# Optimization experiments

Measured on AMD Instinct MI355X. Metric: run time of the kernel, lower is better.

The kernel has to match this reference:

```python
import jax, jax.numpy as jnp
import numpy as np

B, T, D = 16, 2048, 64
K = 8192


def setup_inputs() -> dict:
    key = jax.random.key(0)
    k_x, k_cb = jax.random.split(key)
    x = jax.random.normal(k_x, (B, T, D), dtype=jnp.float32)
    # codebook initialized as randn(K, D) / sqrt(D), as in EMAQuantizer.__init__
    codebook = jax.random.normal(k_cb, (K, D), dtype=jnp.float32) / jnp.sqrt(jnp.float32(D))
    return {"x": x, "codebook": codebook}


def reference(x, codebook):
    """EMAQuantizer.forward (eval mode): nearest-codebook lookup + straight-through.

    x: [B, T, D], codebook: [K, D] -> (x_q_st [B,T,D], indices [B,T])
    """
    orig_shape = x.shape
    x_flat = x.reshape(-1, x.shape[-1])                       # [N, D]
    x2 = jnp.sum(x_flat * x_flat, axis=1, keepdims=True)      # [N, 1]
    e2 = jnp.sum(codebook * codebook, axis=1)[None, :]        # [1, K]
    xe = x_flat @ codebook.T                                  # [N, K]
    dist = x2 + e2 - 2.0 * xe                                 # [N, K] squared L2
    indices = jnp.argmin(dist, axis=1)                        # [N]
    x_q = codebook[indices].reshape(orig_shape)               # gather lookup
    x_q_st = x + jax.lax.stop_gradient(x_q - x)               # straight-through
    return x_q_st, indices.reshape(orig_shape[:-1])
```

## Files before the change

### kernel.cpp

```cpp
#include <hip/hip_runtime.h>
#include <hip/hip_bf16.h>
#include <math.h>

#define N_ROWS 32768
#define KCODES 8192
#define DDIM 64

typedef __attribute__((ext_vector_type(8))) short bf16x8;
typedef __attribute__((ext_vector_type(4))) float f32x4;

#define O_XBF   0
#define O_QPERM 4194304UL
#define O_X2    5242880UL
#define O_E2    5373952UL
#define O_E2MAX 5406720UL
#define O_SLOTS 5668880UL
#define WS_NEEDED (O_SLOTS + (size_t)N_ROWS * 16 * 4)
#define CAPL 32

__device__ __forceinline__ unsigned short f2bf(float f) {
    __hip_bfloat16 h = __float2bfloat16(f);
    union { __hip_bfloat16 b; unsigned short u; } u;
    u.b = h;
    return u.u;
}

__device__ __forceinline__ float bf2f(unsigned short u) {
    return __uint_as_float(((unsigned int)u) << 16);
}

__global__ __launch_bounds__(256) void prep_kernel(const float* __restrict__ x,
                                                   const float* __restrict__ cb,
                                                   unsigned short* __restrict__ xbf,
                                                   uint4* __restrict__ qperm,
                                                   float* __restrict__ x2,
                                                   float* __restrict__ e2,
                                                   int* __restrict__ e2max_bits) {
#pragma clang fp contract(off)
    __shared__ float xrow[64][68];

    const int tid = threadIdx.x;
    const int rloc = tid >> 2;
    const int q4 = tid & 3;
    const int grow = blockIdx.x * 64 + rloc;
    const bool iscb = (grow >= N_ROWS);
    const int r = iscb ? (grow - N_ROWS) : grow;
    const float* src = iscb ? (cb + (size_t)r * DDIM) : (x + (size_t)r * DDIM);

    float4 v[4];
#pragma unroll
    for (int h2 = 0; h2 < 4; ++h2) v[h2] = ((const float4*)src)[q4 * 4 + h2];
#pragma unroll
    for (int h2 = 0; h2 < 4; ++h2)
        *(float4*)&xrow[rloc][q4 * 16 + h2 * 4] = v[h2];

    uint4 ch[2];
#pragma unroll
    for (int hh = 0; hh < 2; ++hh) {
        float4 v0 = v[hh * 2];
        float4 v1 = v[hh * 2 + 1];
        ushort4 a, b;
        a.x = f2bf(v0.x); a.y = f2bf(v0.y); a.z = f2bf(v0.z); a.w = f2bf(v0.w);
        b.x = f2bf(v1.x); b.y = f2bf(v1.y); b.z = f2bf(v1.z); b.w = f2bf(v1.w);
        union { struct { ushort4 lo, hi; } s; uint4 u; } pk;
        pk.s.lo = a; pk.s.hi = b;
        ch[hh] = pk.u;
    }
    if (!iscb) {
        uint4* dst = (uint4*)(xbf + (size_t)r * DDIM);
        dst[q4 * 2 + 0] = ch[0];
        dst[q4 * 2 + 1] = ch[1];
    } else {
        const int g = r >> 4, l15 = r & 15;
#pragma unroll
        for (int hh = 0; hh < 2; ++hh) {
            const int h = q4 * 2 + hh;
            const int slot = (g * 2 + (h >> 2)) * 64 + (h & 3) * 16 + l15;
            qperm[slot] = ch[hh];
        }
    }
    __syncthreads();

    if (tid < 64) {
        float acc[8];
#pragma unroll
        for (int j = 0; j < 8; ++j) { float vv = xrow[tid][j]; acc[j] = vv * vv; }
#pragma unroll
        for (int i = 8; i < 64; i += 8)
#pragma unroll
            for (int j = 0; j < 8; ++j) { float vv = xrow[tid][i + j]; acc[j] = acc[j] + vv * vv; }
        float s = ((acc[0] + acc[1]) + (acc[2] + acc[3])) + ((acc[4] + acc[5]) + (acc[6] + acc[7]));
        const int grow2 = blockIdx.x * 64 + tid;
        if (grow2 < N_ROWS) {
            x2[grow2] = s;
        } else {
            e2[grow2 - N_ROWS] = s;
            float wm = s;
#pragma unroll
            for (int m = 1; m < 64; m <<= 1) wm = fmaxf(wm, __shfl_xor(wm, m, 64));
            if (tid == 0) atomicMax(e2max_bits, __float_as_int(wm));
        }
    }
}

__global__ __launch_bounds__(512) void screen_fused_kernel(
    const unsigned short* __restrict__ xbf, const uint4* __restrict__ qperm,
    const float* __restrict__ xg, const float* __restrict__ cbg,
    const float* __restrict__ x2g, const float* __restrict__ e2g,
    const int* __restrict__ e2max_bits, float* __restrict__ out) {
    __shared__ float tilemax_lds[64 * 64];
    __shared__ unsigned short xs_lds[64][64];
    __shared__ unsigned int wl[4096];
    __shared__ float thr_lds[64];
    __shared__ int cnt_lds[64];
    __shared__ int slots_lds[64][CAPL];
    __shared__ int wcnt;

    const int tid = threadIdx.x;
    const int w = tid >> 6;
    const int lane = tid & 63;
    const int l15 = lane & 15;
    const int quad = lane >> 4;
    const int row0 = blockIdx.x * 64;
    const int T0 = w * 64;

    ((uint4*)xs_lds)[tid] = *((const uint4*)(xbf + (size_t)row0 * DDIM) + tid);
    if (tid == 0) wcnt = 0;
    if (tid < 64) cnt_lds[tid] = 0;

    bf16x8 afrag[4][2];
#pragma unroll
    for (int rt = 0; rt < 4; ++rt)
#pragma unroll
        for (int s = 0; s < 2; ++s)
            afrag[rt][s] = *(const bf16x8*)(xbf + (size_t)(row0 + rt * 16 + l15) * DDIM +
                                            s * 32 + quad * 8);

    const uint4* pB = qperm + (size_t)T0 * 128 + lane;
    const float* pE = e2g + T0 * 16 + l15;

    bf16x8 b0[2], b1[2];
    float ee2[2];
#pragma unroll
    for (int i = 0; i < 2; ++i) {
        b0[i] = *(const bf16x8*)(pB + (size_t)i * 128);
        b1[i] = *(const bf16x8*)(pB + (size_t)i * 128 + 64);
        ee2[i] = pE[i * 16];
    }

    float tmax[4][4];
#pragma unroll
    for (int rt = 0; rt < 4; ++rt)
#pragma unroll
        for (int reg = 0; reg < 4; ++reg) tmax[rt][reg] = -3.0e38f;

    for (int g = 0; g < 8; ++g) {
#pragma unroll 2
        for (int j = 0; j < 8; ++j) {
            const int t = g * 8 + j;
            const int buf = t & 1;
            const bf16x8 B0 = b0[buf];
            const bf16x8 B1 = b1[buf];
            const float eh = -0.5f * ee2[buf];
            if (t < 62) {
                const uint4* p = pB + (size_t)(t + 2) * 128;
                b0[buf] = *(const bf16x8*)p;
                b1[buf] = *(const bf16x8*)(p + 64);
                ee2[buf] = pE[(t + 2) * 16];
            }
            const f32x4 cin = {eh, eh, eh, eh};
#pragma unroll
            for (int rt = 0; rt < 4; ++rt) {
                f32x4 acc = __builtin_amdgcn_mfma_f32_16x16x32_bf16(afrag[rt][0], B0, cin, 0, 0, 0);
                acc = __builtin_amdgcn_mfma_f32_16x16x32_bf16(afrag[rt][1], B1, acc, 0, 0, 0);
#pragma unroll
                for (int reg = 0; reg < 4; ++reg)
                    tmax[rt][reg] = fmaxf(tmax[rt][reg], acc[reg]);
            }
        }
        const int gidx = w * 8 + g;
#pragma unroll
        for (int rt = 0; rt < 4; ++rt)
#pragma unroll
            for (int reg = 0; reg < 4; ++reg) {
                float v = tmax[rt][reg];
                v = fmaxf(v, __shfl_xor(v, 1, 64));
                v = fmaxf(v, __shfl_xor(v, 2, 64));
                v = fmaxf(v, __shfl_xor(v, 4, 64));
                v = fmaxf(v, __shfl_xor(v, 8, 64));
                if (l15 == 0) tilemax_lds[gidx * 64 + rt * 16 + quad * 4 + reg] = v;
                tmax[rt][reg] = -3.0e38f;
            }
    }
    __syncthreads();

    if (tid < 64) {
        float gs = -3.0e38f;
        for (int e = 0; e < 64; ++e) gs = fmaxf(gs, tilemax_lds[e * 64 + tid]);
        const float e2max = __int_as_float(*e2max_bits);
        thr_lds[tid] = gs - 0.005f * sqrtf(x2g[row0 + tid] * e2max) - 0.01f;
    }
    __syncthreads();

    for (int idx = tid; idx < 4096; idx += 512) {
        if (tilemax_lds[idx] >= thr_lds[idx & 63]) {
            int pos = atomicAdd(&wcnt, 1);
            wl[pos] = (unsigned int)idx;
        }
    }
    __syncthreads();

    const int nwl = wcnt;
    for (int p = w; p < nwl; p += 8) {
        const unsigned int e = wl[p];
        const int r = (int)(e & 63u);
        const int g = (int)(e >> 6);
        const float thr_r = thr_lds[r];
#pragma unroll
        for (int hh = 0; hh < 2; ++hh) {
            const int c = g * 128 + hh * 64 + lane;
            float s = -0.5f * e2g[c];
            const int cg = c >> 4, cl = c & 15;
#pragma unroll
            for (int h = 0; h < 8; ++h) {
                const int slot = (cg * 2 + (h >> 2)) * 64 + (h & 3) * 16 + cl;
                union { uint4 u; unsigned short us[8]; } qd, xd;
                qd.u = qperm[slot];
                xd.u = *(const uint4*)&xs_lds[r][h * 8];
#pragma unroll
                for (int k = 0; k < 8; ++k)
                    s = fmaf(bf2f(xd.us[k]), bf2f(qd.us[k]), s);
            }
            if (s >= thr_r) {
                int pos = atomicAdd(&cnt_lds[r], 1);
                if (pos < CAPL) slots_lds[r][pos] = c;
            }
        }
    }
    __syncthreads();

    const int sub = lane >> 3;
    const int ln8 = lane & 7;
    const int r = w * 8 + sub;
    const int row = row0 + r;
    const int c = cnt_lds[r];
    const float x2v = x2g[row];
    const float4* xv4 = (const float4*)(xg + (size_t)row * DDIM);

    float bv = 3.0e38f;
    int bi = 0x7fffffff;
    if (c <= CAPL) {
        for (int i = ln8; i < c; i += 8) {
            int code = slots_lds[r][i];
            float xe = 0.0f;
            const float4* e4 = (const float4*)(cbg + (size_t)code * DDIM);
#pragma unroll
            for (int q = 0; q < 16; ++q) {
                float4 xv = xv4[q];
                float4 ev = e4[q];
                xe = fmaf(xv.x, ev.x, xe);
                xe = fmaf(xv.y, ev.y, xe);
                xe = fmaf(xv.z, ev.z, xe);
                xe = fmaf(xv.w, ev.w, xe);
            }
            float ts = x2v + e2g[code];
            float dist = fmaf(-2.0f, xe, ts);
            if (dist < bv || (dist == bv && code < bi)) { bv = dist; bi = code; }
        }
    } else {
        for (int code = ln8; code < KCODES; code += 8) {
            float xe = 0.0f;
            const float4* e4 = (const float4*)(cbg + (size_t)code * DDIM);
#pragma unroll
            for (int q = 0; q < 16; ++q) {
                float4 xv = xv4[q];
                float4 ev = e4[q];
                xe = fmaf(xv.x, ev.x, xe);
                xe = fmaf(xv.y, ev.y, xe);
                xe = fmaf(xv.z, ev.z, xe);
                xe = fmaf(xv.w, ev.w, xe);
            }
            float ts = x2v + e2g[code];
            float dist = fmaf(-2.0f, xe, ts);
            if (dist < bv || (dist == bv && code < bi)) { bv = dist; bi = code; }
        }
    }
#pragma unroll
    for (int m = 1; m < 8; m <<= 1) {
        float ov = __shfl_xor(bv, m, 64);
        int oi = __shfl_xor(bi, m, 64);
        if (ov < bv || (ov == bv && oi < bi)) { bv = ov; bi = oi; }
    }
    {
        const float4* qs4 = (const float4*)(cbg + (size_t)bi * DDIM);
        float4* os4 = (float4*)(out + (size_t)row * DDIM);
#pragma unroll
        for (int i = 0; i < 2; ++i) {
            float4 xv = xv4[ln8 * 2 + i];
            float4 qv = qs4[ln8 * 2 + i];
            float4 ov;
            ov.x = xv.x + (qv.x - xv.x);
            ov.y = xv.y + (qv.y - xv.y);
            ov.z = xv.z + (qv.z - xv.z);
            ov.w = xv.w + (qv.w - xv.w);
            os4[ln8 * 2 + i] = ov;
        }
        if (ln8 == 0) out[(size_t)N_ROWS * DDIM + row] = (float)bi;
    }
}

#define SPLITK 4
#define KPER (KCODES / SPLITK)
#define TM 128
#define TKT 128
#define NTILES (KPER / TKT)
#define LDSX 132
#define LDSE 132

__global__ __launch_bounds__(256) void sumsq_kernel(const float* __restrict__ x,
                                                    const float* __restrict__ cb,
                                                    float* __restrict__ ws) {
#pragma clang fp contract(off)
    int t = blockIdx.x * 256 + threadIdx.x;
    const float* src;
    float* dst;
    if (t < KCODES) { src = cb + (size_t)t * DDIM; dst = ws + t; }
    else { int r = t - KCODES; src = x + (size_t)r * DDIM; dst = ws + KCODES + r; }
    float acc[8];
#pragma unroll
    for (int j = 0; j < 8; ++j) { float v = src[j]; acc[j] = v * v; }
#pragma unroll
    for (int i = 8; i < 64; i += 8)
#pragma unroll
        for (int j = 0; j < 8; ++j) { float v = src[i + j]; acc[j] = acc[j] + v * v; }
    *dst = ((acc[0] + acc[1]) + (acc[2] + acc[3])) + ((acc[4] + acc[5]) + (acc[6] + acc[7]));
}

__global__ __launch_bounds__(256) void dist_argmin_kernel(const float* __restrict__ x,
                                                          const float* __restrict__ cb,
                                                          const float* __restrict__ e2g,
                                                          const float* __restrict__ x2g,
                                                          float2* __restrict__ partial) {
    __shared__ float smem[DDIM * LDSX + DDIM * LDSE];
    float* Xs = smem;
    float* Es = smem + DDIM * LDSX;
    const int tid = threadIdx.x;
    const int row0 = blockIdx.x * TM;
    const int code0 = blockIdx.y * KPER;
    const int tr = tid >> 4, tc = tid & 15;
    for (int i = tid; i < TM * 16; i += 256) {
        int r = i >> 4, q = i & 15;
        float4 v = ((const float4*)(x + (size_t)(row0 + r) * DDIM))[q];
        Xs[(4 * q + 0) * LDSX + r] = v.x; Xs[(4 * q + 1) * LDSX + r] = v.y;
        Xs[(4 * q + 2) * LDSX + r] = v.z; Xs[(4 * q + 3) * LDSX + r] = v.w;
    }
    float x2v[8];
#pragma unroll
    for (int j = 0; j < 8; ++j) x2v[j] = x2g[row0 + tr * 8 + j];
    float bestV[8]; int bestI[8];
#pragma unroll
    for (int j = 0; j < 8; ++j) { bestV[j] = 3.0e38f; bestI[j] = 0; }
    for (int t = 0; t < NTILES; ++t) {
        __syncthreads();
        const int cbase = code0 + t * TKT;
        for (int i = tid; i < TKT * 16; i += 256) {
            int c = i >> 4, q = i & 15;
            float4 v = ((const float4*)(cb + (size_t)(cbase + c) * DDIM))[q];
            Es[(4 * q + 0) * LDSE + c] = v.x; Es[(4 * q + 1) * LDSE + c] = v.y;
            Es[(4 * q + 2) * LDSE + c] = v.z; Es[(4 * q + 3) * LDSE + c] = v.w;
        }
        __syncthreads();
        float acc[8][8];
#pragma unroll
        for (int a = 0; a < 8; ++a)
#pragma unroll
            for (int b = 0; b < 8; ++b) acc[a][b] = 0.0f;
#pragma unroll 4
        for (int d = 0; d < DDIM; ++d) {
            float xv[8], ev[8];
            float4 xa = *(const float4*)&Xs[d * LDSX + tr * 8];
            float4 xb = *(const float4*)&Xs[d * LDSX + tr * 8 + 4];
            float4 ea = *(const float4*)&Es[d * LDSE + tc * 8];
            float4 eb = *(const float4*)&Es[d * LDSE + tc * 8 + 4];
            xv[0] = xa.x; xv[1] = xa.y; xv[2] = xa.z; xv[3] = xa.w;
            xv[4] = xb.x; xv[5] = xb.y; xv[6] = xb.z; xv[7] = xb.w;
            ev[0] = ea.x; ev[1] = ea.y; ev[2] = ea.z; ev[3] = ea.w;
            ev[4] = eb.x; ev[5] = eb.y; ev[6] = eb.z; ev[7] = eb.w;
#pragma unroll
            for (int a = 0; a < 8; ++a)
#pragma unroll
                for (int b = 0; b < 8; ++b) acc[a][b] = fmaf(xv[a], ev[b], acc[a][b]);
        }
#pragma unroll
        for (int b = 0; b < 8; ++b) {
            int ci = cbase + tc * 8 + b;
            float e2 = e2g[ci];
#pragma unroll
            for (int a = 0; a < 8; ++a) {
                float ts = x2v[a] + e2;
                float dist = fmaf(-2.0f, acc[a][b], ts);
                if (dist < bestV[a]) { bestV[a] = dist; bestI[a] = ci; }
            }
        }
    }
    __syncthreads();
    float* redV = Es;
    int* redI = (int*)(Es + TM * 16);
#pragma unroll
    for (int a = 0; a < 8; ++a) {
        redV[(tr * 8 + a) * 16 + tc] = bestV[a];
        redI[(tr * 8 + a) * 16 + tc] = bestI[a];
    }
    __syncthreads();
    if (tid < TM) {
        float bv = redV[tid * 16];
        int bi = redI[tid * 16];
#pragma unroll
        for (int c = 1; c < 16; ++c) {
            float v = redV[tid * 16 + c];
            int ii = redI[tid * 16 + c];
            if (v < bv || (v == bv && ii < bi)) { bv = v; bi = ii; }
        }
        partial[(size_t)(row0 + tid) * SPLITK + blockIdx.y] = make_float2(bv, __int_as_float(bi));
    }
}

__global__ __launch_bounds__(256) void finalize_kernel(const float2* __restrict__ partial,
                                                       const float* __restrict__ x,
                                                       const float* __restrict__ cb,
                                                       float* __restrict__ out) {
    int t = blockIdx.x * 256 + threadIdx.x;
    int r = t >> 2, j = t & 3;
    float2 p = partial[(size_t)r * SPLITK];
    float bv = p.x;
    int bi = __float_as_int(p.y);
#pragma unroll
    for (int k = 1; k < SPLITK; ++k) {
        float2 q = partial[(size_t)r * SPLITK + k];
        int qi = __float_as_int(q.y);
        if (q.x < bv || (q.x == bv && qi < bi)) { bv = q.x; bi = qi; }
    }
    const float4* xs = (const float4*)(x + (size_t)r * DDIM);
    const float4* qs = (const float4*)(cb + (size_t)bi * DDIM);
    float4* os = (float4*)(out + (size_t)r * DDIM);
#pragma unroll
    for (int i = 0; i < 4; ++i) {
        float4 xv = xs[j * 4 + i];
        float4 qv = qs[j * 4 + i];
        float4 ov;
        ov.x = xv.x + (qv.x - xv.x); ov.y = xv.y + (qv.y - xv.y);
        ov.z = xv.z + (qv.z - xv.z); ov.w = xv.w + (qv.w - xv.w);
        os[j * 4 + i] = ov;
    }
    if (j == 0) out[(size_t)N_ROWS * DDIM + r] = (float)bi;
}

extern "C" void kernel_launch(void* const* d_in, const int* in_sizes, int n_in,
                              void* d_out, int out_size, void* d_ws, size_t ws_size,
                              hipStream_t stream) {
    const float* x = (const float*)d_in[0];
    const float* cb = (const float*)d_in[1];
    float* out = (float*)d_out;

    if (ws_size >= WS_NEEDED) {
        unsigned char* ws = (unsigned char*)d_ws;
        unsigned short* xbf = (unsigned short*)(ws + O_XBF);
        uint4* qperm = (uint4*)(ws + O_QPERM);
        float* x2 = (float*)(ws + O_X2);
        float* e2 = (float*)(ws + O_E2);
        int* e2max_bits = (int*)(ws + O_E2MAX);

        prep_kernel<<<(N_ROWS + KCODES) / 64, 256, 0, stream>>>(x, cb, xbf, qperm, x2, e2,
                                                                e2max_bits);
        screen_fused_kernel<<<N_ROWS / 64, 512, 0, stream>>>(xbf, qperm, x, cb, x2, e2,
                                                             e2max_bits, out);
    } else {
        float* ws = (float*)d_ws;
        float* e2 = ws;
        float* x2 = ws + KCODES;
        float2* partial = (float2*)(ws + KCODES + N_ROWS);
        sumsq_kernel<<<(KCODES + N_ROWS) / 256, 256, 0, stream>>>(x, cb, ws);
        dim3 grid(N_ROWS / TM, SPLITK);
        dist_argmin_kernel<<<grid, 256, 0, stream>>>(x, cb, e2, x2, partial);
        finalize_kernel<<<(N_ROWS * 4) / 256, 256, 0, stream>>>(partial, x, cb, out);
    }
}
```

Measured before the change: 140.4 us.

## Fuse prep and screening into one cooperative kernel with a grid sync

Merges the codebook/row preprocessing and the bf16 MFMA screen-then-rescore kernel into a single cooperative launch. Each block converts its own 64 input rows to bf16 in LDS and computes their squared norms locally. It also converts one 16-code slice of the codebook and stores it in global memory, then a grid-wide sync makes the whole converted codebook visible to all blocks. This removes the second kernel launch and the global round trip of the bf16 copy of x and its norms. In exchange it adds a grid barrier and requires all 512 blocks of 512 threads to be co-resident, falling back to the old two-kernel path if the cooperative launch fails.

```diff
diff --git a/kernel.cpp b/kernel.cpp
--- a/kernel.cpp
+++ b/kernel.cpp
@@ -1,6 +1,9 @@
 #include <hip/hip_runtime.h>
 #include <hip/hip_bf16.h>
+#include <hip/hip_cooperative_groups.h>
 #include <math.h>
+
+namespace cg = cooperative_groups;
 
 #define N_ROWS 32768
 #define KCODES 8192
@@ -27,6 +30,276 @@
 
 __device__ __forceinline__ float bf2f(unsigned short u) {
     return __uint_as_float(((unsigned int)u) << 16);
+}
+
+__global__ __launch_bounds__(512) void vq_fused_kernel(
+    const float* __restrict__ xg, const float* __restrict__ cbg,
+    uint4* __restrict__ qperm, float* __restrict__ e2g,
+    int* __restrict__ e2max_bits, float* __restrict__ out) {
+#pragma clang fp contract(off)
+    __shared__ float tilemax_lds[64 * 64];
+    __shared__ unsigned short xs_lds[64][64];
+    __shared__ unsigned int wl[4096];
+    __shared__ float thr_lds[64];
+    __shared__ float x2_lds[64];
+    __shared__ int cnt_lds[64];
+    __shared__ int slots_lds[64][CAPL];
+    __shared__ int wcnt;
+
+    const int tid = threadIdx.x;
+    const int w = tid >> 6;
+    const int lane = tid & 63;
+    const int l15 = lane & 15;
+    const int quad = lane >> 4;
+    const int row0 = blockIdx.x * 64;
+    const int T0 = w * 64;
+
+    if (tid == 0) wcnt = 0;
+    if (tid < 64) cnt_lds[tid] = 0;
+
+    {
+        const int r0 = tid >> 3;
+        const int h0 = tid & 7;
+        const float* src = xg + (size_t)(row0 + r0) * DDIM + h0 * 8;
+        float4 v0 = ((const float4*)src)[0];
+        float4 v1 = ((const float4*)src)[1];
+        ushort4 a, b;
+        a.x = f2bf(v0.x); a.y = f2bf(v0.y); a.z = f2bf(v0.z); a.w = f2bf(v0.w);
+        b.x = f2bf(v1.x); b.y = f2bf(v1.y); b.z = f2bf(v1.z); b.w = f2bf(v1.w);
+        union { struct { ushort4 lo, hi; } s; uint4 u; } pk;
+        pk.s.lo = a; pk.s.hi = b;
+        *(uint4*)&xs_lds[r0][h0 * 8] = pk.u;
+
+        float sq[8] = {v0.x * v0.x, v0.y * v0.y, v0.z * v0.z, v0.w * v0.w,
+                       v1.x * v1.x, v1.y * v1.y, v1.z * v1.z, v1.w * v1.w};
+        const int base = lane & ~7;
+        float acc[8];
+#pragma unroll
+        for (int j = 0; j < 8; ++j) acc[j] = __shfl(sq[j], base, 64);
+#pragma unroll
+        for (int m = 1; m < 8; ++m)
+#pragma unroll
+            for (int j = 0; j < 8; ++j) acc[j] = acc[j] + __shfl(sq[j], base + m, 64);
+        float s = ((acc[0] + acc[1]) + (acc[2] + acc[3])) +
+                  ((acc[4] + acc[5]) + (acc[6] + acc[7]));
+        if (h0 == 0) x2_lds[r0] = s;
+    }
+
+    if (tid < 128) {
+        const int c = tid >> 3;
+        const int h = tid & 7;
+        const int code = blockIdx.x * 16 + c;
+        const float* src = cbg + (size_t)code * DDIM + h * 8;
+        float4 v0 = ((const float4*)src)[0];
+        float4 v1 = ((const float4*)src)[1];
+        ushort4 a, b;
+        a.x = f2bf(v0.x); a.y = f2bf(v0.y); a.z = f2bf(v0.z); a.w = f2bf(v0.w);
+        b.x = f2bf(v1.x); b.y = f2bf(v1.y); b.z = f2bf(v1.z); b.w = f2bf(v1.w);
+        union { struct { ushort4 lo, hi; } s; uint4 u; } pk;
+        pk.s.lo = a; pk.s.hi = b;
+        const int slot = (blockIdx.x * 2 + (h >> 2)) * 64 + (h & 3) * 16 + c;
+        qperm[slot] = pk.u;
+
+        float sq[8] = {v0.x * v0.x, v0.y * v0.y, v0.z * v0.z, v0.w * v0.w,
+                       v1.x * v1.x, v1.y * v1.y, v1.z * v1.z, v1.w * v1.w};
+        const int base = lane & ~7;
+        float acc[8];
+#pragma unroll
+        for (int j = 0; j < 8; ++j) acc[j] = __shfl(sq[j], base, 64);
+#pragma unroll
+        for (int m = 1; m < 8; ++m)
+#pragma unroll
+            for (int j = 0; j < 8; ++j) acc[j] = acc[j] + __shfl(sq[j], base + m, 64);
+        float s = ((acc[0] + acc[1]) + (acc[2] + acc[3])) +
+                  ((acc[4] + acc[5]) + (acc[6] + acc[7]));
+        if (h == 0) e2g[code] = s;
+        float wm = s;
+#pragma unroll
+        for (int m = 1; m < 64; m <<= 1) wm = fmaxf(wm, __shfl_xor(wm, m, 64));
+        if (lane == 0) atomicMax(e2max_bits, __float_as_int(wm));
+    }
+
+    __threadfence();
+    cg::this_grid().sync();
+
+    bf16x8 afrag[4][2];
+#pragma unroll
+    for (int rt = 0; rt < 4; ++rt)
+#pragma unroll
+        for (int s = 0; s < 2; ++s)
+            afrag[rt][s] = *(const bf16x8*)&xs_lds[rt * 16 + l15][s * 32 + quad * 8];
+
+    const uint4* pB = qperm + (size_t)T0 * 128 + lane;
+    const float* pE = e2g + T0 * 16 + l15;
+
+    bf16x8 b0[2], b1[2];
+    float ee2[2];
+#pragma unroll
+    for (int i = 0; i < 2; ++i) {
+        b0[i] = *(const bf16x8*)(pB + (size_t)i * 128);
+        b1[i] = *(const bf16x8*)(pB + (size_t)i * 128 + 64);
+        ee2[i] = pE[i * 16];
+    }
+
+    float tmax[4][4];
+#pragma unroll
+    for (int rt = 0; rt < 4; ++rt)
+#pragma unroll
+        for (int reg = 0; reg < 4; ++reg) tmax[rt][reg] = -3.0e38f;
+
+    for (int g = 0; g < 8; ++g) {
+#pragma unroll 2
+        for (int j = 0; j < 8; ++j) {
+            const int t = g * 8 + j;
+            const int buf = t & 1;
+            const bf16x8 B0 = b0[buf];
+            const bf16x8 B1 = b1[buf];
+            const float eh = -0.5f * ee2[buf];
+            if (t < 62) {
+                const uint4* p = pB + (size_t)(t + 2) * 128;
+                b0[buf] = *(const bf16x8*)p;
+                b1[buf] = *(const bf16x8*)(p + 64);
+                ee2[buf] = pE[(t + 2) * 16];
+            }
+            const f32x4 cin = {eh, eh, eh, eh};
+#pragma unroll
+            for (int rt = 0; rt < 4; ++rt) {
+                f32x4 acc = __builtin_amdgcn_mfma_f32_16x16x32_bf16(afrag[rt][0], B0, cin, 0, 0, 0);
+                acc = __builtin_amdgcn_mfma_f32_16x16x32_bf16(afrag[rt][1], B1, acc, 0, 0, 0);
+#pragma unroll
+                for (int reg = 0; reg < 4; ++reg)
+                    tmax[rt][reg] = fmaxf(tmax[rt][reg], acc[reg]);
+            }
+        }
+        const int gidx = w * 8 + g;
+#pragma unroll
+        for (int rt = 0; rt < 4; ++rt)
+#pragma unroll
+            for (int reg = 0; reg < 4; ++reg) {
+                float v = tmax[rt][reg];
+                v = fmaxf(v, __shfl_xor(v, 1, 64));
+                v = fmaxf(v, __shfl_xor(v, 2, 64));
+                v = fmaxf(v, __shfl_xor(v, 4, 64));
+                v = fmaxf(v, __shfl_xor(v, 8, 64));
+                if (l15 == 0) tilemax_lds[gidx * 64 + rt * 16 + quad * 4 + reg] = v;
+                tmax[rt][reg] = -3.0e38f;
+            }
+    }
+    __syncthreads();
+
+    if (tid < 64) {
+        float gs = -3.0e38f;
+        for (int e = 0; e < 64; ++e) gs = fmaxf(gs, tilemax_lds[e * 64 + tid]);
+        const float e2max = __int_as_float(*e2max_bits);
+        thr_lds[tid] = gs - 0.005f * sqrtf(x2_lds[tid] * e2max) - 0.01f;
+    }
+    __syncthreads();
+
+    for (int idx = tid; idx < 4096; idx += 512) {
+        if (tilemax_lds[idx] >= thr_lds[idx & 63]) {
+            int pos = atomicAdd(&wcnt, 1);
+            wl[pos] = (unsigned int)idx;
+        }
+    }
+    __syncthreads();
+
+    const int nwl = wcnt;
+    for (int p = w; p < nwl; p += 8) {
+        const unsigned int e = wl[p];
+        const int r = (int)(e & 63u);
+        const int g = (int)(e >> 6);
+        const float thr_r = thr_lds[r];
+#pragma unroll
+        for (int hh = 0; hh < 2; ++hh) {
+            const int c = g * 128 + hh * 64 + lane;
+            float s = -0.5f * e2g[c];
+            const int cg = c >> 4, cl = c & 15;
+#pragma unroll
+            for (int h = 0; h < 8; ++h) {
+                const int slot = (cg * 2 + (h >> 2)) * 64 + (h & 3) * 16 + cl;
+                union { uint4 u; unsigned short us[8]; } qd, xd;
+                qd.u = qperm[slot];
+                xd.u = *(const uint4*)&xs_lds[r][h * 8];
+#pragma unroll
+                for (int k = 0; k < 8; ++k)
+                    s = fmaf(bf2f(xd.us[k]), bf2f(qd.us[k]), s);
+            }
+            if (s >= thr_r) {
+                int pos = atomicAdd(&cnt_lds[r], 1);
+                if (pos < CAPL) slots_lds[r][pos] = c;
+            }
+        }
+    }
+    __syncthreads();
+
+    const int sub = lane >> 3;
+    const int ln8 = lane & 7;
+    const int r = w * 8 + sub;
+    const int row = row0 + r;
+    const int c = cnt_lds[r];
+    const float x2v = x2_lds[r];
+    const float4* xv4 = (const float4*)(xg + (size_t)row * DDIM);
+
+    float bv = 3.0e38f;
+    int bi = 0x7fffffff;
+    if (c <= CAPL) {
+        for (int i = ln8; i < c; i += 8) {
+            int code = slots_lds[r][i];
+            float xe = 0.0f;
+            const float4* e4 = (const float4*)(cbg + (size_t)code * DDIM);
+#pragma unroll
+            for (int q = 0; q < 16; ++q) {
+                float4 xv = xv4[q];
+                float4 ev = e4[q];
+                xe = fmaf(xv.x, ev.x, xe);
+                xe = fmaf(xv.y, ev.y, xe);
+                xe = fmaf(xv.z, ev.z, xe);
+                xe = fmaf(xv.w, ev.w, xe);
+            }
+            float ts = x2v + e2g[code];
+            float dist = fmaf(-2.0f, xe, ts);
+            if (dist < bv || (dist == bv && code < bi)) { bv = dist; bi = code; }
+        }
+    } else {
+        for (int code = ln8; code < KCODES; code += 8) {
+            float xe = 0.0f;
+            const float4* e4 = (const float4*)(cbg + (size_t)code * DDIM);
+#pragma unroll
+            for (int q = 0; q < 16; ++q) {
+                float4 xv = xv4[q];
+                float4 ev = e4[q];
+                xe = fmaf(xv.x, ev.x, xe);
+                xe = fmaf(xv.y, ev.y, xe);
+                xe = fmaf(xv.z, ev.z, xe);
+                xe = fmaf(xv.w, ev.w, xe);
+            }
+            float ts = x2v + e2g[code];
+            float dist = fmaf(-2.0f, xe, ts);
+            if (dist < bv || (dist == bv && code < bi)) { bv = dist; bi = code; }
+        }
+    }
+#pragma unroll
+    for (int m = 1; m < 8; m <<= 1) {
+        float ov = __shfl_xor(bv, m, 64);
+        int oi = __shfl_xor(bi, m, 64);
+        if (ov < bv || (ov == bv && oi < bi)) { bv = ov; bi = oi; }
+    }
+    {
+        const float4* qs4 = (const float4*)(cbg + (size_t)bi * DDIM);
+        float4* os4 = (float4*)(out + (size_t)row * DDIM);
+#pragma unroll
+        for (int i = 0; i < 2; ++i) {
+            float4 xv = xv4[ln8 * 2 + i];
+            float4 qv = qs4[ln8 * 2 + i];
+            float4 ov;
+            ov.x = xv.x + (qv.x - xv.x);
+            ov.y = xv.y + (qv.y - xv.y);
+            ov.z = xv.z + (qv.z - xv.z);
+            ov.w = xv.w + (qv.w - xv.w);
+            os4[ln8 * 2 + i] = ov;
+        }
+        if (ln8 == 0) out[(size_t)N_ROWS * DDIM + row] = (float)bi;
+    }
 }
 
 __global__ __launch_bounds__(256) void prep_kernel(const float* __restrict__ x,
@@ -470,10 +743,17 @@
         float* e2 = (float*)(ws + O_E2);
         int* e2max_bits = (int*)(ws + O_E2MAX);
 
-        prep_kernel<<<(N_ROWS + KCODES) / 64, 256, 0, stream>>>(x, cb, xbf, qperm, x2, e2,
-                                                                e2max_bits);
-        screen_fused_kernel<<<N_ROWS / 64, 512, 0, stream>>>(xbf, qperm, x, cb, x2, e2,
-                                                             e2max_bits, out);
+        void* args[] = {(void*)&x, (void*)&cb, (void*)&qperm, (void*)&e2,
+                        (void*)&e2max_bits, (void*)&out};
+        hipError_t err = hipLaunchCooperativeKernel((const void*)vq_fused_kernel,
+                                                    dim3(N_ROWS / 64), dim3(512),
+                                                    args, 0, stream);
+        if (err != hipSuccess) {
+            prep_kernel<<<(N_ROWS + KCODES) / 64, 256, 0, stream>>>(x, cb, xbf, qperm, x2,
+                                                                    e2, e2max_bits);
+            screen_fused_kernel<<<N_ROWS / 64, 512, 0, stream>>>(xbf, qperm, x, cb, x2, e2,
+                                                                 e2max_bits, out);
+        }
     } else {
         float* ws = (float*)d_ws;
         float* e2 = ws;
```

Result: slower. 254.6 us (+81.3%).

## Fuse x bf16 conversion and row norms into screen kernel; add MFMA priority

Applied to the files above, without the earlier changes.

The prep kernel now handles only the codebook. The screen kernel converts its own 64 x rows to bf16 in LDS, computes x2 with wave shuffles, and reads the MFMA A-fragments from LDS rather than a global bf16 copy. This removes the xbf/x2 workspace round trip and shrinks the prep launch, at the cost of a little extra work and a barrier at the start of the main kernel. It also raises wave priority with s_setprio around the MFMA loop.

```diff
diff --git a/kernel.cpp b/kernel.cpp
--- a/kernel.cpp
+++ b/kernel.cpp
@@ -29,23 +29,18 @@
     return __uint_as_float(((unsigned int)u) << 16);
 }
 
-__global__ __launch_bounds__(256) void prep_kernel(const float* __restrict__ x,
-                                                   const float* __restrict__ cb,
-                                                   unsigned short* __restrict__ xbf,
-                                                   uint4* __restrict__ qperm,
-                                                   float* __restrict__ x2,
-                                                   float* __restrict__ e2,
-                                                   int* __restrict__ e2max_bits) {
+__global__ __launch_bounds__(256) void prep_cb_kernel(const float* __restrict__ cb,
+                                                      uint4* __restrict__ qperm,
+                                                      float* __restrict__ e2,
+                                                      int* __restrict__ e2max_bits) {
 #pragma clang fp contract(off)
     __shared__ float xrow[64][68];
 
     const int tid = threadIdx.x;
     const int rloc = tid >> 2;
     const int q4 = tid & 3;
-    const int grow = blockIdx.x * 64 + rloc;
-    const bool iscb = (grow >= N_ROWS);
-    const int r = iscb ? (grow - N_ROWS) : grow;
-    const float* src = iscb ? (cb + (size_t)r * DDIM) : (x + (size_t)r * DDIM);
+    const int r = blockIdx.x * 64 + rloc;
+    const float* src = cb + (size_t)r * DDIM;
 
     float4 v[4];
 #pragma unroll
@@ -66,11 +61,7 @@
         pk.s.lo = a; pk.s.hi = b;
         ch[hh] = pk.u;
     }
-    if (!iscb) {
-        uint4* dst = (uint4*)(xbf + (size_t)r * DDIM);
-        dst[q4 * 2 + 0] = ch[0];
-        dst[q4 * 2 + 1] = ch[1];
-    } else {
+    {
         const int g = r >> 4, l15 = r & 15;
 #pragma unroll
         for (int hh = 0; hh < 2; ++hh) {
@@ -90,28 +81,24 @@
 #pragma unroll
             for (int j = 0; j < 8; ++j) { float vv = xrow[tid][i + j]; acc[j] = acc[j] + vv * vv; }
         float s = ((acc[0] + acc[1]) + (acc[2] + acc[3])) + ((acc[4] + acc[5]) + (acc[6] + acc[7]));
-        const int grow2 = blockIdx.x * 64 + tid;
-        if (grow2 < N_ROWS) {
-            x2[grow2] = s;
-        } else {
-            e2[grow2 - N_ROWS] = s;
-            float wm = s;
-#pragma unroll
-            for (int m = 1; m < 64; m <<= 1) wm = fmaxf(wm, __shfl_xor(wm, m, 64));
-            if (tid == 0) atomicMax(e2max_bits, __float_as_int(wm));
-        }
+        e2[blockIdx.x * 64 + tid] = s;
+        float wm = s;
+#pragma unroll
+        for (int m = 1; m < 64; m <<= 1) wm = fmaxf(wm, __shfl_xor(wm, m, 64));
+        if (tid == 0) atomicMax(e2max_bits, __float_as_int(wm));
     }
 }
 
 __global__ __launch_bounds__(512) void screen_fused_kernel(
-    const unsigned short* __restrict__ xbf, const uint4* __restrict__ qperm,
     const float* __restrict__ xg, const float* __restrict__ cbg,
-    const float* __restrict__ x2g, const float* __restrict__ e2g,
+    const uint4* __restrict__ qperm, const float* __restrict__ e2g,
     const int* __restrict__ e2max_bits, float* __restrict__ out) {
+#pragma clang fp contract(off)
     __shared__ float tilemax_lds[64 * 64];
     __shared__ unsigned short xs_lds[64][64];
     __shared__ unsigned int wl[4096];
     __shared__ float thr_lds[64];
+    __shared__ float x2_lds[64];
     __shared__ int cnt_lds[64];
     __shared__ int slots_lds[64][CAPL];
     __shared__ int wcnt;
@@ -124,17 +111,44 @@
     const int row0 = blockIdx.x * 64;
     const int T0 = w * 64;
 
-    ((uint4*)xs_lds)[tid] = *((const uint4*)(xbf + (size_t)row0 * DDIM) + tid);
     if (tid == 0) wcnt = 0;
     if (tid < 64) cnt_lds[tid] = 0;
 
+    {
+        const int r0 = tid >> 3;
+        const int h0 = tid & 7;
+        const float* src = xg + (size_t)(row0 + r0) * DDIM + h0 * 8;
+        float4 v0 = ((const float4*)src)[0];
+        float4 v1 = ((const float4*)src)[1];
+        ushort4 a, b;
+        a.x = f2bf(v0.x); a.y = f2bf(v0.y); a.z = f2bf(v0.z); a.w = f2bf(v0.w);
+        b.x = f2bf(v1.x); b.y = f2bf(v1.y); b.z = f2bf(v1.z); b.w = f2bf(v1.w);
+        union { struct { ushort4 lo, hi; } s; uint4 u; } pk;
+        pk.s.lo = a; pk.s.hi = b;
+        *(uint4*)&xs_lds[r0][h0 * 8] = pk.u;
+
+        float sq[8] = {v0.x * v0.x, v0.y * v0.y, v0.z * v0.z, v0.w * v0.w,
+                       v1.x * v1.x, v1.y * v1.y, v1.z * v1.z, v1.w * v1.w};
+        const int base = lane & ~7;
+        float acc[8];
+#pragma unroll
+        for (int j = 0; j < 8; ++j) acc[j] = __shfl(sq[j], base, 64);
+#pragma unroll
+        for (int m = 1; m < 8; ++m)
+#pragma unroll
+            for (int j = 0; j < 8; ++j) acc[j] = acc[j] + __shfl(sq[j], base + m, 64);
+        float s = ((acc[0] + acc[1]) + (acc[2] + acc[3])) +
+                  ((acc[4] + acc[5]) + (acc[6] + acc[7]));
+        if (h0 == 0) x2_lds[r0] = s;
+    }
+    __syncthreads();
+
     bf16x8 afrag[4][2];
 #pragma unroll
     for (int rt = 0; rt < 4; ++rt)
 #pragma unroll
         for (int s = 0; s < 2; ++s)
-            afrag[rt][s] = *(const bf16x8*)(xbf + (size_t)(row0 + rt * 16 + l15) * DDIM +
-                                            s * 32 + quad * 8);
+            afrag[rt][s] = *(const bf16x8*)&xs_lds[rt * 16 + l15][s * 32 + quad * 8];
 
     const uint4* pB = qperm + (size_t)T0 * 128 + lane;
     const float* pE = e2g + T0 * 16 + l15;
@@ -169,6 +183,7 @@
                 ee2[buf] = pE[(t + 2) * 16];
             }
             const f32x4 cin = {eh, eh, eh, eh};
+            __builtin_amdgcn_s_setprio(1);
 #pragma unroll
             for (int rt = 0; rt < 4; ++rt) {
                 f32x4 acc = __builtin_amdgcn_mfma_f32_16x16x32_bf16(afrag[rt][0], B0, cin, 0, 0, 0);
@@ -177,6 +192,7 @@
                 for (int reg = 0; reg < 4; ++reg)
                     tmax[rt][reg] = fmaxf(tmax[rt][reg], acc[reg]);
             }
+            __builtin_amdgcn_s_setprio(0);
         }
         const int gidx = w * 8 + g;
 #pragma unroll
@@ -198,7 +214,7 @@
         float gs = -3.0e38f;
         for (int e = 0; e < 64; ++e) gs = fmaxf(gs, tilemax_lds[e * 64 + tid]);
         const float e2max = __int_as_float(*e2max_bits);
-        thr_lds[tid] = gs - 0.005f * sqrtf(x2g[row0 + tid] * e2max) - 0.01f;
+        thr_lds[tid] = gs - 0.005f * sqrtf(x2_lds[tid] * e2max) - 0.01f;
     }
     __syncthreads();
 
@@ -244,7 +260,7 @@
     const int r = w * 8 + sub;
     const int row = row0 + r;
     const int c = cnt_lds[r];
-    const float x2v = x2g[row];
+    const float x2v = x2_lds[r];
     const float4* xv4 = (const float4*)(xg + (size_t)row * DDIM);
 
     float bv = 3.0e38f;
@@ -464,15 +480,12 @@
 
     if (ws_size >= WS_NEEDED) {
         unsigned char* ws = (unsigned char*)d_ws;
-        unsigned short* xbf = (unsigned short*)(ws + O_XBF);
         uint4* qperm = (uint4*)(ws + O_QPERM);
-        float* x2 = (float*)(ws + O_X2);
         float* e2 = (float*)(ws + O_E2);
         int* e2max_bits = (int*)(ws + O_E2MAX);
 
-        prep_kernel<<<(N_ROWS + KCODES) / 64, 256, 0, stream>>>(x, cb, xbf, qperm, x2, e2,
-                                                                e2max_bits);
-        screen_fused_kernel<<<N_ROWS / 64, 512, 0, stream>>>(xbf, qperm, x, cb, x2, e2,
+        prep_cb_kernel<<<KCODES / 64, 256, 0, stream>>>(cb, qperm, e2, e2max_bits);
+        screen_fused_kernel<<<N_ROWS / 64, 512, 0, stream>>>(x, cb, qperm, e2,
                                                              e2max_bits, out);
     } else {
         float* ws = (float*)d_ws;
```

New measurement: 138.2 us. About the same (-1.6%).
